# Performance work log

Hardware: AMD Instinct MI355X
Metric: run time of the kernel (lower is better)

## Reference

```python
import jax, jax.numpy as jnp
import numpy as np

B, K, C, O = 8, 100000, 16, 16
HG, WG = 512, 512
ALPHA_PRIOR = 1.0
KERN = np.array([[0.075, 0.125, 0.075], [0.125, 0.3, 0.125], [0.075, 0.125, 0.075]], dtype=np.float32)


def setup_inputs() -> dict:
    key = jax.random.key(0)
    k1, k2, k3, k4, k5 = jax.random.split(key, 5)
    node_feat = jax.random.normal(k1, (B, K, C), dtype=jnp.float32)
    node_xy = jax.random.uniform(k2, (B, K, 2), dtype=jnp.float32, minval=0.0, maxval=WG - 1.0)
    node_types = jax.random.randint(k3, (B, K), 0, 2)
    # kaiming_normal_ fan_out: std = sqrt(2 / fan_out), fan_out = O*1*1
    std = (2.0 / O) ** 0.5
    w_obj = jax.random.normal(k4, (O, C), dtype=jnp.float32) * std
    w_prior = jax.random.normal(k5, (O, C), dtype=jnp.float32) * std
    hw = np.array([HG, WG], dtype=np.int64)
    return {"node_feat": node_feat, "node_xy": node_xy, "hw": hw,
            "node_types": node_types, "w_obj": w_obj, "w_prior": w_prior}


def rasterize(node_feat, node_xy, weight, H, W):
    # node_feat [B,K,C], node_xy [B,K,2], weight [B,K] 0/1 mask (masked scatter == scatter of zeros)
    xs = jnp.clip(jnp.round(node_xy[..., 0]), 0, W - 1).astype(jnp.int32)
    ys = jnp.clip(jnp.round(node_xy[..., 1]), 0, H - 1).astype(jnp.int32)
    idx = ys * W + xs  # [B,K] flat grid index
    src = node_feat * weight[..., None]  # zero out non-selected nodes

    def scat(idx_b, src_b):
        return jnp.zeros((H * W, src_b.shape[-1]), src_b.dtype).at[idx_b].add(src_b)

    grid = jax.vmap(scat)(idx, src)  # [B,HW,C]
    return grid.reshape(grid.shape[0], H, W, -1).transpose(0, 3, 1, 2)  # [B,C,H,W]


def splat3x3(x, kern):
    # depthwise 3x3 conv, groups = C
    c = x.shape[1]
    w = jnp.broadcast_to(kern[None, None], (c, 1, 3, 3))
    return jax.lax.conv_general_dilated(
        x, w, window_strides=(1, 1), padding='SAME',
        dimension_numbers=('NCHW', 'OIHW', 'NCHW'), feature_group_count=c)


def reference(node_feat, node_xy, hw, node_types, w_obj, w_prior):
    H, W = int(hw[0]), int(hw[1])
    kern = jnp.asarray(KERN)
    mask_obj = (node_types == 0).astype(node_feat.dtype)
    mask_prior = (node_types == 1).astype(node_feat.dtype)
    map_obj = splat3x3(rasterize(node_feat, node_xy, mask_obj, H, W), kern)
    map_prior = splat3x3(rasterize(node_feat, node_xy, mask_prior, H, W), kern)
    # rasterize + splat run under torch.no_grad() in the original
    map_obj = jax.lax.stop_gradient(map_obj)
    map_prior = jax.lax.stop_gradient(map_prior)
    out = jnp.einsum('oc,bchw->bohw', w_obj, map_obj) \
        + ALPHA_PRIOR * jnp.einsum('oc,bchw->bohw', w_prior, map_prior)
    return out
```

## Files before the change

### kernel.cpp

```cpp
#include <hip/hip_runtime.h>

#define B_ 8
#define K_ 100000
#define NODES (B_ * K_)
#define C_ 16
#define O_ 16
#define H_ 512
#define W_ 512
#define TSX 32
#define TSY 16
#define NTX (W_ / TSX)
#define NTY (H_ / TSY)
#define NBKT (B_ * NTX * NTY)
#define CAP 512
#define EX (TSX + 2)
#define EY (TSY + 2)
#define PLANE (EX * EY)

#define FB 1000
#define FPB (FB / B_)
#define FCHUNK (K_ / FPB)

#define CURP 16
#define CUR_BYTES (NBKT * CURP * 4)
#define IDS_OFF CUR_BYTES
#define P_OFF (IDS_OFF + NBKT * CAP * 4)
#define WS_NEED_PRE ((size_t)P_OFF + (size_t)NODES * O_ * 4)
#define WS_NEED_MIN ((size_t)P_OFF)

__device__ __forceinline__ float bf_lo(unsigned int u) {
    union { unsigned int i; float f; } v; v.i = u << 16; return v.f;
}
__device__ __forceinline__ float bf_hi(unsigned int u) {
    union { unsigned int i; float f; } v; v.i = u & 0xffff0000u; return v.f;
}
__device__ __forceinline__ unsigned short f2bf(float f) {
    union { float f; unsigned int u; } v; v.f = f;
    unsigned int u = v.u;
    u += 0x7fffu + ((u >> 16) & 1u);
    return (unsigned short)(u >> 16);
}

__device__ __forceinline__ int probe_fp32_ballot(const unsigned int* xy) {
    const int lane = threadIdx.x & 63;
    int bad = 0;
    #pragma unroll
    for (int k = 0; k < 4; ++k) {
        float lo = bf_lo(xy[lane + (k << 6)]);
        bad |= !(lo >= 0.0f && lo <= 512.0f);
    }
    return __ballot(bad) != 0ull;
}

__device__ __forceinline__ void decode_xy(const void* xy, int fp32, int n,
                                          int& xs, int& ys)
{
    float x, y;
    if (fp32) { float2 p = ((const float2*)xy)[n]; x = p.x; y = p.y; }
    else { unsigned int u = ((const unsigned int*)xy)[n]; x = bf_lo(u); y = bf_hi(u); }
    xs = min(max((int)rintf(x), 0), W_ - 1);
    ys = min(max((int)rintf(y), 0), H_ - 1);
}

__device__ __forceinline__ void load_feat16(const void* feat, size_t n, int fp32,
                                            float* f)
{
    if (fp32) {
        const float4* ff = (const float4*)feat + n * 4;
        float4 a = ff[0], b2 = ff[1], c = ff[2], d = ff[3];
        f[0]=a.x; f[1]=a.y; f[2]=a.z; f[3]=a.w;
        f[4]=b2.x; f[5]=b2.y; f[6]=b2.z; f[7]=b2.w;
        f[8]=c.x; f[9]=c.y; f[10]=c.z; f[11]=c.w;
        f[12]=d.x; f[13]=d.y; f[14]=d.z; f[15]=d.w;
    } else {
        const uint4* ff = (const uint4*)feat + n * 2;
        uint4 A = ff[0], Bv = ff[1];
        f[0]=bf_lo(A.x);  f[1]=bf_hi(A.x);  f[2]=bf_lo(A.y);  f[3]=bf_hi(A.y);
        f[4]=bf_lo(A.z);  f[5]=bf_hi(A.z);  f[6]=bf_lo(A.w);  f[7]=bf_hi(A.w);
        f[8]=bf_lo(Bv.x); f[9]=bf_hi(Bv.x); f[10]=bf_lo(Bv.y); f[11]=bf_hi(Bv.y);
        f[12]=bf_lo(Bv.z); f[13]=bf_hi(Bv.z); f[14]=bf_lo(Bv.w); f[15]=bf_hi(Bv.w);
    }
}

__device__ __forceinline__ void load_weights_lds(float* wl, int fp32,
                                                 const void* w_obj,
                                                 const void* w_prior,
                                                 int tid, int nthreads)
{
    for (int i = tid; i < 2 * O_ * C_; i += nthreads) {
        if (fp32) {
            wl[i] = (i < O_ * C_) ? ((const float*)w_obj)[i]
                                  : ((const float*)w_prior)[i - O_ * C_];
        } else {
            unsigned short raw = (i < O_ * C_)
                ? ((const unsigned short*)w_obj)[i]
                : ((const unsigned short*)w_prior)[i - O_ * C_];
            union { unsigned int u; float f; } v; v.u = ((unsigned int)raw) << 16;
            wl[i] = v.f;
        }
    }
}

template<bool PRE>
__global__ __launch_bounds__(256) void fill_bins(
    const void* __restrict__ feat, const void* __restrict__ xy,
    const int* __restrict__ types,
    const void* __restrict__ w_obj, const void* __restrict__ w_prior,
    int* __restrict__ cursor, int* __restrict__ ids, float* __restrict__ p)
{
    __shared__ int hist[NTX * NTY];
    __shared__ unsigned int rec[FCHUNK];
    __shared__ float wl[PRE ? 2 * O_ * C_ : 2];

    const int tid = threadIdx.x;
    const int fp32 = probe_fp32_ballot((const unsigned int*)xy);
    for (int j = tid; j < NTX * NTY; j += 256) hist[j] = 0;
    if constexpr (PRE) load_weights_lds(wl, fp32, w_obj, w_prior, tid, 256);
    __syncthreads();

    const int bb = blockIdx.x / FPB;
    const int local0 = (blockIdx.x % FPB) * FCHUNK;
    const int s = bb * K_ + local0;

    for (int ii = tid; ii < FCHUNK; ii += 256) {
        const int n = s + ii;
        int xs, ys; decode_xy(xy, fp32, n, xs, ys);
        const int t = (types[n] != 0);
        rec[ii] = (unsigned)(xs | (ys << 9) | (t << 18));

        if constexpr (PRE) {
            float f[16];
            load_feat16(feat, (size_t)n, fp32, f);
            const float* wrow = &wl[t * O_ * C_];
            float pv[16];
            #pragma unroll
            for (int o = 0; o < O_; ++o) {
                float acc = 0.f;
                #pragma unroll
                for (int c = 0; c < C_; ++c) acc = fmaf(wrow[o * C_ + c], f[c], acc);
                pv[o] = acc;
            }
            float4* pout = (float4*)(p + (size_t)n * O_);
            pout[0] = make_float4(pv[0],  pv[1],  pv[2],  pv[3]);
            pout[1] = make_float4(pv[4],  pv[5],  pv[6],  pv[7]);
            pout[2] = make_float4(pv[8],  pv[9],  pv[10], pv[11]);
            pout[3] = make_float4(pv[12], pv[13], pv[14], pv[15]);
        }

        int xlo = max((xs - 1) >> 5, 0), xhi = min((xs + 1) >> 5, NTX - 1);
        int ylo = max((ys - 1) >> 4, 0), yhi = min((ys + 1) >> 4, NTY - 1);
        for (int tyy = ylo; tyy <= yhi; ++tyy)
            for (int txx = xlo; txx <= xhi; ++txx)
                atomicAdd(&hist[tyy * NTX + txx], 1);
    }
    __syncthreads();

    for (int j = tid; j < NTX * NTY; j += 256) {
        int c = hist[j];
        hist[j] = c ? atomicAdd(&cursor[(bb * NTX * NTY + j) * CURP], c) : 0;
    }
    __syncthreads();

    for (int ii = tid; ii < FCHUNK; ii += 256) {
        unsigned r = rec[ii];
        int xs = r & 511, ys = (r >> 9) & 511, t = (r >> 18) & 1;
        int local = local0 + ii;
        int xlo = max((xs - 1) >> 5, 0), xhi = min((xs + 1) >> 5, NTX - 1);
        int ylo = max((ys - 1) >> 4, 0), yhi = min((ys + 1) >> 4, NTY - 1);
        for (int tyy = ylo; tyy <= yhi; ++tyy)
            for (int txx = xlo; txx <= xhi; ++txx) {
                int bk = tyy * NTX + txx;
                int slot = atomicAdd(&hist[bk], 1);
                if (slot < CAP) {
                    int lx = xs - (txx << 5) + 1;
                    int ly = ys - (tyy << 4) + 1;
                    ids[(bb * NTX * NTY + bk) * CAP + slot] =
                        local | (t << 17) | (lx << 18) | (ly << 24);
                }
            }
    }
}

template<bool PRE>
__global__ __launch_bounds__(512) void tile_fused(
    const void* __restrict__ src ,
    const void* __restrict__ xy,
    const void* __restrict__ w_obj, const void* __restrict__ w_prior,
    const int* __restrict__ cursor, const int* __restrict__ ids,
    void* __restrict__ out)
{
    __shared__ float accs[O_ * PLANE];
    __shared__ float wl[PRE ? 2 : 2 * O_ * C_];

    const int tid = threadIdx.x;
    const int tx = blockIdx.x, ty = blockIdx.y, b = blockIdx.z;
    const int bucket = (b * NTY + ty) * NTX + tx;
    int cnt = cursor[bucket * CURP];
    if (cnt > CAP) cnt = CAP;
    const int fp32 = probe_fp32_ballot((const unsigned int*)xy);

    const int node = ((tid & 7) << 6) | (tid >> 3);
    const bool active = (node < cnt);
    float f[16];
    int t = 0, lx = 0, ly = 0;
    if (active) {
        const unsigned pck = (unsigned)ids[bucket * CAP + node];
        const int local = pck & 0x1FFFF;
        t  = (pck >> 17) & 1;
        lx = (pck >> 18) & 63;
        ly = (pck >> 24) & 31;
        const size_t n = (size_t)b * K_ + local;
        if constexpr (PRE) {
            const float4* pp = (const float4*)src + n * 4;
            float4 a = pp[0], b2 = pp[1], c = pp[2], d = pp[3];
            f[0]=a.x; f[1]=a.y; f[2]=a.z; f[3]=a.w;
            f[4]=b2.x; f[5]=b2.y; f[6]=b2.z; f[7]=b2.w;
            f[8]=c.x; f[9]=c.y; f[10]=c.z; f[11]=c.w;
            f[12]=d.x; f[13]=d.y; f[14]=d.z; f[15]=d.w;
        } else {
            load_feat16(src, n, fp32, f);
        }
    }

    for (int i = tid; i < O_ * PLANE; i += 512) accs[i] = 0.f;
    if constexpr (!PRE) load_weights_lds(wl, fp32, w_obj, w_prior, tid, 512);
    __syncthreads();

    if (active) {
        float* cell = &accs[ly * EX + lx];
        if constexpr (PRE) {
            #pragma unroll
            for (int o = 0; o < O_; ++o) atomicAdd(cell + o * PLANE, f[o]);
        } else {
            const float* wrow = &wl[t * O_ * C_];
            #pragma unroll
            for (int o = 0; o < O_; ++o) {
                float acc = 0.f;
                #pragma unroll
                for (int c = 0; c < C_; ++c) acc = fmaf(wrow[o * C_ + c], f[c], acc);
                atomicAdd(cell + o * PLANE, acc);
            }
        }
    }
    __syncthreads();

    const int x = tid & 31;
    const int o = tid >> 5;
    const float* pl = &accs[o * PLANE + x];
    float hA2 = 0.f, hA1 = 0.f, hB1 = 0.f;
    const int x0 = tx * TSX, y0 = ty * TSY;
    const size_t obase = (((size_t)(b * O_ + o)) * H_) * W_;

    #pragma unroll
    for (int iy = 0; iy < EY; ++iy) {
        float l = pl[iy * EX], c = pl[iy * EX + 1], r = pl[iy * EX + 2];
        float sfx = l + r;
        float hA = fmaf(0.075f, sfx, 0.125f * c);
        float hB = fmaf(0.125f, sfx, 0.3f * c);
        if (iy >= 2) {
            float v = hA2 + hB1 + hA;
            size_t oi = obase + (size_t)(y0 + iy - 2) * W_ + (x0 + x);
            if (fp32) __builtin_nontemporal_store(v, (float*)out + oi);
            else      __builtin_nontemporal_store(f2bf(v), (unsigned short*)out + oi);
        }
        hA2 = hA1; hA1 = hA; hB1 = hB;
    }
}

extern "C" void kernel_launch(void* const* d_in, const int* in_sizes, int n_in,
                              void* d_out, int out_size, void* d_ws, size_t ws_size,
                              hipStream_t stream)
{
    const void* feat = d_in[0];
    const void* xy = d_in[1];
    const int* types = (const int*)d_in[3];
    const void* w_obj = d_in[4];
    const void* w_prior = d_in[5];

    int* cursor = (int*)d_ws;
    int* ids = (int*)((char*)d_ws + IDS_OFF);
    float* p = (float*)((char*)d_ws + P_OFF);

    hipMemsetAsync(cursor, 0, CUR_BYTES, stream);
    if (ws_size >= WS_NEED_PRE) {
        fill_bins<true><<<FB, 256, 0, stream>>>(feat, xy, types, w_obj, w_prior,
                                                cursor, ids, p);
        tile_fused<true><<<dim3(NTX, NTY, B_), 512, 0, stream>>>(
            p, xy, w_obj, w_prior, cursor, ids, d_out);
    } else {
        fill_bins<false><<<FB, 256, 0, stream>>>(feat, xy, types, w_obj, w_prior,
                                                 cursor, ids, p);
        tile_fused<false><<<dim3(NTX, NTY, B_), 512, 0, stream>>>(
            feat, xy, w_obj, w_prior, cursor, ids, d_out);
    }
}
```

Before: 303.1 us.

## Process four tiles per block with prefetch of next tile's node gathers

Result: no change. 300.3 us (-0.9%).

```diff
diff --git a/kernel.cpp b/kernel.cpp
--- a/kernel.cpp
+++ b/kernel.cpp
@@ -17,16 +17,18 @@
 #define EY (TSY + 2)
 #define PLANE (EX * EY)
 
-#define FB 1000
+#define FB 2000
 #define FPB (FB / B_)
 #define FCHUNK (K_ / FPB)
+
+#define TPB 4
+#define TGRID (NBKT / TPB)
 
 #define CURP 16
 #define CUR_BYTES (NBKT * CURP * 4)
 #define IDS_OFF CUR_BYTES
 #define P_OFF (IDS_OFF + NBKT * CAP * 4)
 #define WS_NEED_PRE ((size_t)P_OFF + (size_t)NODES * O_ * 4)
-#define WS_NEED_MIN ((size_t)P_OFF)
 
 __device__ __forceinline__ float bf_lo(unsigned int u) {
     union { unsigned int i; float f; } v; v.i = u << 16; return v.f;
@@ -79,6 +81,22 @@
         f[4]=bf_lo(A.z);  f[5]=bf_hi(A.z);  f[6]=bf_lo(A.w);  f[7]=bf_hi(A.w);
         f[8]=bf_lo(Bv.x); f[9]=bf_hi(Bv.x); f[10]=bf_lo(Bv.y); f[11]=bf_hi(Bv.y);
         f[12]=bf_lo(Bv.z); f[13]=bf_hi(Bv.z); f[14]=bf_lo(Bv.w); f[15]=bf_hi(Bv.w);
+    }
+}
+
+template<bool PRE>
+__device__ __forceinline__ void gather16(const void* src, size_t n, int fp32,
+                                         float* f)
+{
+    if constexpr (PRE) {
+        const float4* pp = (const float4*)src + n * 4;
+        float4 a = pp[0], b2 = pp[1], c = pp[2], d = pp[3];
+        f[0]=a.x; f[1]=a.y; f[2]=a.z; f[3]=a.w;
+        f[4]=b2.x; f[5]=b2.y; f[6]=b2.z; f[7]=b2.w;
+        f[8]=c.x; f[9]=c.y; f[10]=c.z; f[11]=c.w;
+        f[12]=d.x; f[13]=d.y; f[14]=d.z; f[15]=d.w;
+    } else {
+        load_feat16(src, n, fp32, f);
     }
 }
 
@@ -182,7 +200,7 @@
 }
 
 template<bool PRE>
-__global__ __launch_bounds__(512) void tile_fused(
+__global__ __launch_bounds__(512) void tile_persist(
     const void* __restrict__ src ,
     const void* __restrict__ xy,
     const void* __restrict__ w_obj, const void* __restrict__ w_prior,
@@ -193,77 +211,89 @@
     __shared__ float wl[PRE ? 2 : 2 * O_ * C_];
 
     const int tid = threadIdx.x;
-    const int tx = blockIdx.x, ty = blockIdx.y, b = blockIdx.z;
-    const int bucket = (b * NTY + ty) * NTX + tx;
-    int cnt = cursor[bucket * CURP];
+    const int fp32 = probe_fp32_ballot((const unsigned int*)xy);
+    if constexpr (!PRE) load_weights_lds(wl, fp32, w_obj, w_prior, tid, 512);
+
+    const int node = ((tid & 7) << 6) | (tid >> 3);
+    const int t0 = blockIdx.x * TPB;
+
+    int cnt = cursor[t0 * CURP];
+    unsigned pck = (unsigned)ids[t0 * CAP + node];
     if (cnt > CAP) cnt = CAP;
-    const int fp32 = probe_fp32_ballot((const unsigned int*)xy);
-
-    const int node = ((tid & 7) << 6) | (tid >> 3);
-    const bool active = (node < cnt);
     float f[16];
-    int t = 0, lx = 0, ly = 0;
-    if (active) {
-        const unsigned pck = (unsigned)ids[bucket * CAP + node];
-        const int local = pck & 0x1FFFF;
-        t  = (pck >> 17) & 1;
-        lx = (pck >> 18) & 63;
-        ly = (pck >> 24) & 31;
-        const size_t n = (size_t)b * K_ + local;
-        if constexpr (PRE) {
-            const float4* pp = (const float4*)src + n * 4;
-            float4 a = pp[0], b2 = pp[1], c = pp[2], d = pp[3];
-            f[0]=a.x; f[1]=a.y; f[2]=a.z; f[3]=a.w;
-            f[4]=b2.x; f[5]=b2.y; f[6]=b2.z; f[7]=b2.w;
-            f[8]=c.x; f[9]=c.y; f[10]=c.z; f[11]=c.w;
-            f[12]=d.x; f[13]=d.y; f[14]=d.z; f[15]=d.w;
-        } else {
-            load_feat16(src, n, fp32, f);
-        }
-    }
-
-    for (int i = tid; i < O_ * PLANE; i += 512) accs[i] = 0.f;
-    if constexpr (!PRE) load_weights_lds(wl, fp32, w_obj, w_prior, tid, 512);
-    __syncthreads();
-
-    if (active) {
-        float* cell = &accs[ly * EX + lx];
-        if constexpr (PRE) {
-            #pragma unroll
-            for (int o = 0; o < O_; ++o) atomicAdd(cell + o * PLANE, f[o]);
-        } else {
-            const float* wrow = &wl[t * O_ * C_];
-            #pragma unroll
-            for (int o = 0; o < O_; ++o) {
-                float acc = 0.f;
+    if (node < cnt) {
+        const size_t n = (size_t)(t0 >> 9) * K_ + (pck & 0x1FFFF);
+        gather16<PRE>(src, n, fp32, f);
+    }
+
+    #pragma unroll
+    for (int k = 0; k < TPB; ++k) {
+        const int tt = t0 + k;
+        const int b = tt >> 9, ty = (tt >> 4) & 31, tx = tt & 15;
+
+        int cnt_n = 0; unsigned pck_n = 0;
+        if (k + 1 < TPB) {
+            cnt_n = cursor[(tt + 1) * CURP];
+            pck_n = (unsigned)ids[(tt + 1) * CAP + node];
+        }
+
+        for (int i = tid; i < O_ * PLANE; i += 512) accs[i] = 0.f;
+        __syncthreads();
+
+        const bool active = node < cnt;
+        if (active) {
+            const int lx = (pck >> 18) & 63, ly = (pck >> 24) & 31;
+            float* cell = &accs[ly * EX + lx];
+            if constexpr (PRE) {
                 #pragma unroll
-                for (int c = 0; c < C_; ++c) acc = fmaf(wrow[o * C_ + c], f[c], acc);
-                atomicAdd(cell + o * PLANE, acc);
-            }
-        }
-    }
-    __syncthreads();
-
-    const int x = tid & 31;
-    const int o = tid >> 5;
-    const float* pl = &accs[o * PLANE + x];
-    float hA2 = 0.f, hA1 = 0.f, hB1 = 0.f;
-    const int x0 = tx * TSX, y0 = ty * TSY;
-    const size_t obase = (((size_t)(b * O_ + o)) * H_) * W_;
-
-    #pragma unroll
-    for (int iy = 0; iy < EY; ++iy) {
-        float l = pl[iy * EX], c = pl[iy * EX + 1], r = pl[iy * EX + 2];
-        float sfx = l + r;
-        float hA = fmaf(0.075f, sfx, 0.125f * c);
-        float hB = fmaf(0.125f, sfx, 0.3f * c);
-        if (iy >= 2) {
-            float v = hA2 + hB1 + hA;
-            size_t oi = obase + (size_t)(y0 + iy - 2) * W_ + (x0 + x);
-            if (fp32) __builtin_nontemporal_store(v, (float*)out + oi);
-            else      __builtin_nontemporal_store(f2bf(v), (unsigned short*)out + oi);
-        }
-        hA2 = hA1; hA1 = hA; hB1 = hB;
+                for (int o = 0; o < O_; ++o) atomicAdd(cell + o * PLANE, f[o]);
+            } else {
+                const int t = (pck >> 17) & 1;
+                const float* wrow = &wl[t * O_ * C_];
+                #pragma unroll
+                for (int o = 0; o < O_; ++o) {
+                    float acc = 0.f;
+                    #pragma unroll
+                    for (int c = 0; c < C_; ++c)
+                        acc = fmaf(wrow[o * C_ + c], f[c], acc);
+                    atomicAdd(cell + o * PLANE, acc);
+                }
+            }
+        }
+
+        if (k + 1 < TPB) {
+            if (cnt_n > CAP) cnt_n = CAP;
+            if (node < cnt_n) {
+                const size_t n = (size_t)((tt + 1) >> 9) * K_ + (pck_n & 0x1FFFF);
+                gather16<PRE>(src, n, fp32, f);
+            }
+        }
+        __syncthreads();
+
+        const int x = tid & 31;
+        const int o = tid >> 5;
+        const float* pl = &accs[o * PLANE + x];
+        float hA2 = 0.f, hA1 = 0.f, hB1 = 0.f;
+        const int x0 = tx * TSX, y0 = ty * TSY;
+        const size_t obase = (((size_t)(b * O_ + o)) * H_) * W_;
+
+        #pragma unroll
+        for (int iy = 0; iy < EY; ++iy) {
+            float l = pl[iy * EX], c = pl[iy * EX + 1], r = pl[iy * EX + 2];
+            float sfx = l + r;
+            float hA = fmaf(0.075f, sfx, 0.125f * c);
+            float hB = fmaf(0.125f, sfx, 0.3f * c);
+            if (iy >= 2) {
+                float v = hA2 + hB1 + hA;
+                size_t oi = obase + (size_t)(y0 + iy - 2) * W_ + (x0 + x);
+                if (fp32) __builtin_nontemporal_store(v, (float*)out + oi);
+                else      __builtin_nontemporal_store(f2bf(v), (unsigned short*)out + oi);
+            }
+            hA2 = hA1; hA1 = hA; hB1 = hB;
+        }
+
+        __syncthreads();
+        cnt = cnt_n; pck = pck_n;
     }
 }
 
@@ -285,12 +315,12 @@
     if (ws_size >= WS_NEED_PRE) {
         fill_bins<true><<<FB, 256, 0, stream>>>(feat, xy, types, w_obj, w_prior,
                                                 cursor, ids, p);
-        tile_fused<true><<<dim3(NTX, NTY, B_), 512, 0, stream>>>(
+        tile_persist<true><<<TGRID, 512, 0, stream>>>(
             p, xy, w_obj, w_prior, cursor, ids, d_out);
     } else {
         fill_bins<false><<<FB, 256, 0, stream>>>(feat, xy, types, w_obj, w_prior,
                                                  cursor, ids, p);
-        tile_fused<false><<<dim3(NTX, NTY, B_), 512, 0, stream>>>(
+        tile_persist<false><<<TGRID, 512, 0, stream>>>(
             feat, xy, w_obj, w_prior, cursor, ids, d_out);
     }
 }
```
